# Performance work log

Measured on AMD Instinct MI355X. Metric: run time of the kernel, lower is better.

Reference implementation:

```python
import jax, jax.numpy as jnp
import numpy as np

N = 10000
E = 160000
C = 256        # in_channels
M = 256        # mid_channels
R = 64         # nregion


def _glorot(key, shape):
    fan_in, fan_out = shape[-1], shape[0]
    lim = (6.0 / (fan_in + fan_out)) ** 0.5
    return jax.random.uniform(key, shape, jnp.float32, -lim, lim)


def setup_inputs() -> dict:
    key = jax.random.key(0)
    ks = jax.random.split(key, 12)
    x = jax.random.normal(ks[0], (N, C), jnp.float32)
    edge_index = jax.random.randint(ks[1], (2, E), 0, N, jnp.int32)
    conv_w = _glorot(ks[2], (C, C))
    conv_b = jnp.zeros((C,), jnp.float32)
    lin1_w = _glorot(ks[3], (M, C)); lin1_b = jnp.zeros((M,), jnp.float32)
    lin2_w = _glorot(ks[4], (M, M)); lin2_b = jnp.zeros((M,), jnp.float32)
    lin3_w = _glorot(ks[5], (1, M)); lin3_b = jnp.zeros((1,), jnp.float32)
    lin4_w = _glorot(ks[6], (M, M)); lin4_b = jnp.zeros((M,), jnp.float32)
    bilin_w = _glorot(ks[7], (R, M, M)) * 0.1
    bilin_b = jnp.zeros((R,), jnp.float32)
    return {"x": x, "edge_index": edge_index,
            "conv_w": conv_w, "conv_b": conv_b,
            "lin1_w": lin1_w, "lin1_b": lin1_b,
            "lin2_w": lin2_w, "lin2_b": lin2_b,
            "lin3_w": lin3_w, "lin3_b": lin3_b,
            "lin4_w": lin4_w, "lin4_b": lin4_b,
            "bilin_w": bilin_w, "bilin_b": bilin_b}


def gcn_conv(x, edge_index, w, b):
    # PyG GCNConv: add self-loops, symmetric D^-1/2 (A+I) D^-1/2 normalization
    src, dst = edge_index[0], edge_index[1]
    n = x.shape[0]
    xw = x @ w.T                                            # [N, C]
    deg = jnp.ones((n,), xw.dtype).at[dst].add(jnp.ones((E,), xw.dtype))  # +1 for self loop
    dinv = jax.lax.rsqrt(deg)
    norm = dinv[src] * dinv[dst]                            # [E]
    agg = jnp.zeros_like(xw).at[dst].add(norm[:, None] * xw[src])
    agg = agg + (dinv * dinv)[:, None] * xw                 # self-loop messages
    return agg + b


def reference(x, edge_index, conv_w, conv_b, lin1_w, lin1_b, lin2_w, lin2_b,
              lin3_w, lin3_b, lin4_w, lin4_b, bilin_w, bilin_b):
    out = jax.nn.relu(gcn_conv(x, edge_index, conv_w, conv_b))
    x0 = out + x                                            # residual [N, C]
    x0 = jax.nn.relu(x0 @ lin1_w.T + lin1_b)                # [N, M]
    x1 = jax.nn.relu(x0 @ lin2_w.T + lin2_b)
    x1 = x1 @ lin3_w.T + lin3_b                             # [N, 1]
    x2 = jax.nn.relu(x0 @ lin4_w.T + lin4_b)                # [N, M]
    # Bilinear(x2, x2): out[n,r] = x2[n] @ W[r] @ x2[n] + b[r]
    t = (x2 @ bilin_w.reshape(R * M, M).T).reshape(-1, R, M)  # [N, R, M]
    x2 = jnp.sum(t * x2[:, None, :], axis=-1) + bilin_b       # [N, R]
    return (x1, x2)
```

## Files before the change

kernel.cpp:

```cpp
#include <hip/hip_runtime.h>

typedef unsigned short u16;
typedef __attribute__((ext_vector_type(8))) short bf16x8;
typedef __attribute__((ext_vector_type(4))) float f32x4;

#define N_NODES 10000
#define E_EDGES 160000

__device__ __forceinline__ float b2f(u16 u) {
  union { unsigned i; float f; } c; c.i = ((unsigned)u) << 16; return c.f;
}
__device__ __forceinline__ u16 f2b(float f) {
  union { float f; unsigned i; } c; c.f = f;
  unsigned i = c.i;
  return (u16)((i + 0x7FFFu + ((i >> 16) & 1u)) >> 16);
}

__global__ void detect_kernel(const unsigned* __restrict__ w, int* __restrict__ flag) {
  int t = threadIdx.x;
  int cnt = 0;
  for (int i = t; i < 1024; i += 64) {
    unsigned e = (w[i] >> 7) & 0xFF;
    cnt += (e >= 100 && e <= 145) ? 1 : 0;
  }
  for (int o = 32; o; o >>= 1) cnt += __shfl_xor(cnt, o);
  if (t == 0) *flag = (cnt >= 512) ? 1 : 0;
}
__global__ void canon_kernel(const void* __restrict__ src, u16* __restrict__ dst,
                             int n, const int* __restrict__ flag) {
  int i = blockIdx.x * 256 + threadIdx.x;
  if (i >= n) return;
  if (*flag) dst[i] = ((const u16*)src)[i];
  else       dst[i] = f2b(((const float*)src)[i]);
}
__global__ void canon4_kernel(const void* s0, const void* s1, const void* s2, const void* s3,
                              u16* d0, u16* d1, u16* d2, u16* d3,
                              const int* __restrict__ flag) {
  int tsel = blockIdx.x >> 8;
  int i = (blockIdx.x & 255) * 256 + threadIdx.x;
  const void* s = tsel == 0 ? s0 : tsel == 1 ? s1 : tsel == 2 ? s2 : s3;
  u16* d = tsel == 0 ? d0 : tsel == 1 ? d1 : tsel == 2 ? d2 : d3;
  if (*flag) d[i] = ((const u16*)s)[i];
  else       d[i] = f2b(((const float*)s)[i]);
}
__global__ void canon_small_kernel(const void* s0, const void* s1, const void* s2,
                                   const void* s3, const void* s4, const void* s5,
                                   const void* s6,
                                   u16* d0, u16* d1, u16* d2, u16* d3, u16* d4,
                                   u16* d5, u16* d6, const int* __restrict__ flag) {
  int t = threadIdx.x;
  int f = *flag;
  const void* srcs[7] = {s0, s1, s2, s3, s4, s5, s6};
  u16* dsts[7] = {d0, d1, d2, d3, d4, d5, d6};
  const int ns[7] = {256, 256, 256, 256, 256, 64, 1};
#pragma unroll
  for (int k = 0; k < 7; ++k) {
    if (t < ns[k]) {
      if (f) dsts[k][t] = ((const u16*)srcs[k])[t];
      else   dsts[k][t] = f2b(((const float*)srcs[k])[t]);
    }
  }
}

__device__ __forceinline__ void stage_async(const u16* __restrict__ src, int stride,
                                            int row0, int maxRow, int k0,
                                            u16* lds, int w, int lane) {
  int rsel = lane >> 3;
  int gch = (lane & 7) ^ rsel;
#pragma unroll
  for (int i = 0; i < 4; ++i) {
    int rb = (w * 4 + i) * 8;
    int grow = row0 + rb + rsel;
    grow = grow > maxRow ? maxRow : grow;
    const u16* gp = src + (size_t)grow * stride + k0 + gch * 8;
    u16* lp = lds + rb * 64;
    __builtin_amdgcn_global_load_lds(
        (const __attribute__((address_space(1))) void*)gp,
        (__attribute__((address_space(3))) void*)lp, 16, 0, 0);
  }
}

__device__ __forceinline__ void mma_tile(const u16* lA, const u16* lB,
                                         f32x4 acc[4][4], int wr, int wc, int lane) {
#pragma unroll
  for (int ks = 0; ks < 2; ++ks) {
    bf16x8 af[4], bfr[4];
    int g = ks * 4 + (lane >> 4);
#pragma unroll
    for (int t = 0; t < 4; ++t) {
      int rowA = wr * 64 + t * 16 + (lane & 15);
      af[t] = *(const bf16x8*)(lA + rowA * 64 + ((g ^ (rowA & 7)) * 8));
      int rowB = wc * 64 + t * 16 + (lane & 15);
      bfr[t] = *(const bf16x8*)(lB + rowB * 64 + ((g ^ (rowB & 7)) * 8));
    }
#pragma unroll
    for (int ti = 0; ti < 4; ++ti)
#pragma unroll
      for (int tj = 0; tj < 4; ++tj)
        acc[ti][tj] = __builtin_amdgcn_mfma_f32_16x16x32_bf16(af[ti], bfr[tj],
                                                              acc[ti][tj], 0, 0, 0);
  }
}

template <bool RELU, bool F32OUT>
__global__ __launch_bounds__(256, 2)
void gemm_kernel(const u16* __restrict__ A, const u16* __restrict__ B,
                 const u16* __restrict__ bias, float* __restrict__ outF,
                 u16* __restrict__ outB, int NN, int J, int K) {
  __shared__ u16 lA[128 * 64];
  __shared__ u16 lB[128 * 64];
  int lane = threadIdx.x & 63;
  int w = threadIdx.x >> 6;
  int wr = w >> 1, wc = w & 1;
  int n0 = blockIdx.y * 128;
  int j0 = blockIdx.x * 128;
  f32x4 acc[4][4];
#pragma unroll
  for (int i = 0; i < 4; ++i)
#pragma unroll
    for (int j = 0; j < 4; ++j) acc[i][j] = (f32x4){0.f, 0.f, 0.f, 0.f};

  for (int kt = 0; kt < K; kt += 64) {
    stage_async(A, K, n0, NN - 1, kt, lA, w, lane);
    stage_async(B, K, j0, J - 1, kt, lB, w, lane);
    __syncthreads();
    mma_tile(lA, lB, acc, wr, wc, lane);
    __syncthreads();
  }

#pragma unroll
  for (int ti = 0; ti < 4; ++ti)
#pragma unroll
    for (int tj = 0; tj < 4; ++tj) {
      int col = j0 + wc * 64 + tj * 16 + (lane & 15);
      float bv = bias ? b2f(bias[col]) : 0.0f;
#pragma unroll
      for (int r = 0; r < 4; ++r) {
        int row = n0 + wr * 64 + ti * 16 + ((lane >> 4) << 2) + r;
        if (row < NN) {
          float v = acc[ti][tj][r] + bv;
          if (RELU) v = fmaxf(v, 0.0f);
          if (F32OUT) outF[(size_t)row * J + col] = v;
          else        outB[(size_t)row * J + col] = f2b(v);
        }
      }
    }
}

__global__ __launch_bounds__(256, 2)
void gemm_fused234_kernel(const u16* __restrict__ A, const u16* __restrict__ B,
                          const u16* __restrict__ bias, const u16* __restrict__ w3,
                          float* __restrict__ out1acc, u16* __restrict__ x2v, int NN) {
  __shared__ u16 lA[128 * 64];
  __shared__ u16 lB[128 * 64];
  int lane = threadIdx.x & 63;
  int w = threadIdx.x >> 6;
  int wr = w >> 1, wc = w & 1;
  int n0 = blockIdx.y * 128;
  int j0 = blockIdx.x * 128;
  f32x4 acc[4][4];
#pragma unroll
  for (int i = 0; i < 4; ++i)
#pragma unroll
    for (int j = 0; j < 4; ++j) acc[i][j] = (f32x4){0.f, 0.f, 0.f, 0.f};

  for (int kt = 0; kt < 256; kt += 64) {
    stage_async(A, 256, n0, NN - 1, kt, lA, w, lane);
    stage_async(B, 256, j0, 511, kt, lB, w, lane);
    __syncthreads();
    mma_tile(lA, lB, acc, wr, wc, lane);
    __syncthreads();
  }

  if (j0 < 256) {
    float part[4][4];
#pragma unroll
    for (int ti = 0; ti < 4; ++ti)
#pragma unroll
      for (int r = 0; r < 4; ++r) part[ti][r] = 0.0f;
#pragma unroll
    for (int ti = 0; ti < 4; ++ti)
#pragma unroll
      for (int tj = 0; tj < 4; ++tj) {
        int col = j0 + wc * 64 + tj * 16 + (lane & 15);
        float bv = b2f(bias[col]);
        float wv = b2f(w3[col]);
#pragma unroll
        for (int r = 0; r < 4; ++r) {
          float v = fmaxf(acc[ti][tj][r] + bv, 0.0f);
          part[ti][r] += v * wv;
        }
      }
#pragma unroll
    for (int ti = 0; ti < 4; ++ti)
#pragma unroll
      for (int r = 0; r < 4; ++r) {
        float s = part[ti][r];
        s += __shfl_xor(s, 1);
        s += __shfl_xor(s, 2);
        s += __shfl_xor(s, 4);
        s += __shfl_xor(s, 8);
        if ((lane & 15) == 0) {
          int row = n0 + wr * 64 + ti * 16 + ((lane >> 4) << 2) + r;
          if (row < NN) unsafeAtomicAdd(&out1acc[row], s);
        }
      }
  } else {
#pragma unroll
    for (int ti = 0; ti < 4; ++ti)
#pragma unroll
      for (int tj = 0; tj < 4; ++tj) {
        int col = j0 + wc * 64 + tj * 16 + (lane & 15);
        float bv = b2f(bias[col]);
#pragma unroll
        for (int r = 0; r < 4; ++r) {
          int row = n0 + wr * 64 + ti * 16 + ((lane >> 4) << 2) + r;
          if (row < NN) {
            float v = fmaxf(acc[ti][tj][r] + bv, 0.0f);
            x2v[(size_t)row * 256 + (col - 256)] = f2b(v);
          }
        }
      }
  }
}

__global__ __launch_bounds__(256, 2)
void bilinear_kernel(const u16* __restrict__ x2v, const u16* __restrict__ W,
                     float* __restrict__ out2acc, int NN) {
  __shared__ u16 lA[128 * 64];
  __shared__ u16 lB[128 * 64];
  int lane = threadIdx.x & 63;
  int w = threadIdx.x >> 6;
  int wr = w >> 1, wc = w & 1;
  int n0 = blockIdx.y * 128;
  int rm0 = blockIdx.x * 128;
  int m0g = rm0 & 255;
  int xv_kt = (m0g >> 6) + wc;
  f32x4 acc[4][4];
#pragma unroll
  for (int i = 0; i < 4; ++i)
#pragma unroll
    for (int j = 0; j < 4; ++j) acc[i][j] = (f32x4){0.f, 0.f, 0.f, 0.f};

  u16 xvr[4][16];

#pragma unroll
  for (int kt4 = 0; kt4 < 4; ++kt4) {
    stage_async(x2v, 256, n0, NN - 1, kt4 * 64, lA, w, lane);
    stage_async(W, 256, rm0, 16383, kt4 * 64, lB, w, lane);
    __syncthreads();
    mma_tile(lA, lB, acc, wr, wc, lane);
    if (kt4 == xv_kt) {
#pragma unroll
      for (int tj = 0; tj < 4; ++tj) {
        int kl = tj * 16 + (lane & 15);
        int ch = kl >> 3, off = kl & 7;
#pragma unroll
        for (int ti = 0; ti < 4; ++ti)
#pragma unroll
          for (int r = 0; r < 4; ++r) {
            int rowl = wr * 64 + ti * 16 + ((lane >> 4) << 2) + r;
            xvr[tj][ti * 4 + r] = lA[rowl * 64 + ((ch ^ (rowl & 7)) * 8) + off];
          }
      }
    }
    __syncthreads();
  }

  int region = rm0 >> 8;
  float rowsum[4][4];
#pragma unroll
  for (int ti = 0; ti < 4; ++ti)
#pragma unroll
    for (int r = 0; r < 4; ++r) rowsum[ti][r] = 0.0f;

#pragma unroll
  for (int ti = 0; ti < 4; ++ti)
#pragma unroll
    for (int tj = 0; tj < 4; ++tj)
#pragma unroll
      for (int r = 0; r < 4; ++r)
        rowsum[ti][r] += acc[ti][tj][r] * b2f(xvr[tj][ti * 4 + r]);

#pragma unroll
  for (int ti = 0; ti < 4; ++ti)
#pragma unroll
    for (int r = 0; r < 4; ++r) {
      float s = rowsum[ti][r];
      s += __shfl_xor(s, 1);
      s += __shfl_xor(s, 2);
      s += __shfl_xor(s, 4);
      s += __shfl_xor(s, 8);
      if ((lane & 15) == 0) {
        int rowl = wr * 64 + ti * 16 + ((lane >> 4) << 2) + r;
        int n = n0 + rowl;
        if (n < NN) unsafeAtomicAdd(&out2acc[(size_t)n * 64 + region], s);
      }
    }
}

__global__ void hist_kernel(const int* __restrict__ ei, int* __restrict__ count) {
  int i = blockIdx.x * 256 + threadIdx.x;
  if (i < E_EDGES) atomicAdd(&count[ei[E_EDGES + i]], 1);
}

__global__ void scan_kernel(const int* __restrict__ count, int* __restrict__ start,
                            int* __restrict__ cursor, float* __restrict__ dinv) {
  __shared__ int sdata[1024];
  __shared__ int carry_s;
  int t = threadIdx.x;
  if (t == 0) carry_s = 0;
  __syncthreads();
  for (int base = 0; base < N_NODES; base += 1024) {
    int i = base + t;
    int v = (i < N_NODES) ? count[i] : 0;
    sdata[t] = v;
    __syncthreads();
    for (int o = 1; o < 1024; o <<= 1) {
      int u = (t >= o) ? sdata[t - o] : 0;
      __syncthreads();
      sdata[t] += u;
      __syncthreads();
    }
    int excl = sdata[t] - v + carry_s;
    if (i < N_NODES) {
      start[i] = excl;
      cursor[i] = excl;
      dinv[i] = rsqrtf(1.0f + (float)v);
    }
    __syncthreads();
    if (t == 1023) carry_s += sdata[1023];
    __syncthreads();
  }
}

__global__ void place_kernel(const int* __restrict__ ei, int* __restrict__ cursor,
                             int* __restrict__ order) {
  int i = blockIdx.x * 256 + threadIdx.x;
  if (i >= E_EDGES) return;
  int d = ei[E_EDGES + i];
  int pos = atomicAdd(&cursor[d], 1);
  order[pos] = i;
}

__global__ void gather_kernel(const int* __restrict__ ei, const int* __restrict__ order,
                              const int* __restrict__ start, const int* __restrict__ count,
                              const float* __restrict__ dinv, const float* __restrict__ xw,
                              const u16* __restrict__ conv_b, const u16* __restrict__ x,
                              u16* __restrict__ x0) {
  int node = (blockIdx.x * blockDim.x + threadIdx.x) >> 6;
  int lane = threadIdx.x & 63;
  if (node >= N_NODES) return;
  int s0 = start[node], cnt = count[node];
  float dn = dinv[node];
  float ax = 0.f, ay = 0.f, az = 0.f, aw = 0.f;
  for (int base = 0; base < cnt; base += 64) {
    int rem = cnt - base;
    int m = rem < 64 ? rem : 64;
    int eid = (lane < m) ? order[s0 + base + lane] : 0;
    int s = (lane < m) ? ei[eid] : 0;
    float nrm = (lane < m) ? dinv[s] * dn : 0.f;
    for (int j = 0; j < m; ++j) {
      int sj = __shfl(s, j);
      float nj = __shfl(nrm, j);
      float4 v = *((const float4*)(xw + (size_t)sj * 256) + lane);
      ax += nj * v.x; ay += nj * v.y; az += nj * v.z; aw += nj * v.w;
    }
  }
  float4 sv = *((const float4*)(xw + (size_t)node * 256) + lane);
  float slw = dn * dn;
  const u16* bb = conv_b + lane * 4;
  const u16* xr = x + (size_t)node * 256 + lane * 4;
  u16 o[4];
  float vals[4] = {ax + slw * sv.x, ay + slw * sv.y, az + slw * sv.z, aw + slw * sv.w};
#pragma unroll
  for (int j = 0; j < 4; ++j) {
    float v = vals[j] + b2f(bb[j]);
    v = fmaxf(v, 0.0f) + b2f(xr[j]);
    o[j] = f2b(v);
  }
  *((ushort4*)(x0 + (size_t)node * 256) + lane) = make_ushort4(o[0], o[1], o[2], o[3]);
}

__global__ void out_final_kernel(const float* __restrict__ out1acc,
                                 const float* __restrict__ out2acc,
                                 const u16* __restrict__ b3, const u16* __restrict__ bb,
                                 void* __restrict__ dout, const int* __restrict__ flag) {
  int idx = blockIdx.x * 256 + threadIdx.x;
  int f = *flag;
  if (idx < N_NODES) {
    float v = out1acc[idx] + b2f(b3[0]);
    if (f) ((u16*)dout)[idx] = f2b(v);
    else   ((float*)dout)[idx] = v;
  } else if (idx < N_NODES + N_NODES * 64) {
    int k = idx - N_NODES;
    float v = out2acc[k] + b2f(bb[k & 63]);
    if (f) ((u16*)dout)[idx] = f2b(v);
    else   ((float*)dout)[idx] = v;
  }
}

extern "C" void kernel_launch(void* const* d_in, const int* in_sizes, int n_in,
                              void* d_out, int out_size, void* d_ws, size_t ws_size,
                              hipStream_t stream) {
  const int* ei = (const int*)d_in[1];

  float* ws      = (float*)d_ws;
  float* xw      = ws;
  int*   count   = (int*)(xw + N_NODES * 256);
  int*   start   = count + 10240;
  int*   cursor  = start + 10240;
  int*   order   = cursor + 10240;
  float* dinv    = (float*)(order + E_EDGES);
  float* out1acc = dinv + 10240;
  float* out2acc = out1acc + 10240;
  u16* x0  = (u16*)(out2acc + N_NODES * 64);
  u16* x0m = x0 + N_NODES * 256;
  u16* x2v = x0m + N_NODES * 256;
  u16* cx  = x2v + N_NODES * 256;
  u16* cwc = cx + N_NODES * 256;
  u16* cw1 = cwc + 65536;
  u16* cw2 = cw1 + 65536;
  u16* cw4 = cw2 + 65536;
  u16* cwB = cw4 + 65536;
  u16* cbc = cwB + 4194304;
  u16* cb1 = cbc + 256;
  u16* cb2 = cb1 + 256;
  u16* cb4 = cb2 + 256;
  u16* cw3 = cb4 + 256;
  u16* cbB = cw3 + 256;
  u16* cb3 = cbB + 64;
  int* flag = (int*)(cb3 + 16);

  hipMemsetAsync(count, 0, N_NODES * sizeof(int), stream);
  hipMemsetAsync(out1acc, 0, (10240 + (size_t)N_NODES * 64) * sizeof(float), stream);

  detect_kernel<<<1, 64, 0, stream>>>((const unsigned*)d_in[0], flag);

  canon_kernel<<<(N_NODES * 256 + 255) / 256, 256, 0, stream>>>(d_in[0], cx, N_NODES * 256, flag);
  canon4_kernel<<<1024, 256, 0, stream>>>(d_in[2], d_in[4], d_in[6], d_in[10],
                                          cwc, cw1, cw2, cw4, flag);
  canon_small_kernel<<<1, 256, 0, stream>>>(d_in[3], d_in[5], d_in[7], d_in[11],
                                            d_in[8], d_in[13], d_in[9],
                                            cbc, cb1, cb2, cb4, cw3, cbB, cb3, flag);
  canon_kernel<<<(4194304 + 255) / 256, 256, 0, stream>>>(d_in[12], cwB, 4194304, flag);

  hist_kernel<<<(E_EDGES + 255) / 256, 256, 0, stream>>>(ei, count);
  scan_kernel<<<1, 1024, 0, stream>>>(count, start, cursor, dinv);
  place_kernel<<<(E_EDGES + 255) / 256, 256, 0, stream>>>(ei, cursor, order);

  gemm_kernel<false, true><<<dim3(2, 79), 256, 0, stream>>>(
      cx, cwc, nullptr, xw, nullptr, N_NODES, 256, 256);

  gather_kernel<<<(N_NODES * 64 + 255) / 256, 256, 0, stream>>>(
      ei, order, start, count, dinv, xw, cbc, cx, x0);

  gemm_kernel<true, false><<<dim3(2, 79), 256, 0, stream>>>(
      x0, cw1, cb1, nullptr, x0m, N_NODES, 256, 256);

  gemm_fused234_kernel<<<dim3(4, 79), 256, 0, stream>>>(
      x0m, cw2, cb2, cw3, out1acc, x2v, N_NODES);

  bilinear_kernel<<<dim3(128, 79), 256, 0, stream>>>(x2v, cwB, out2acc, N_NODES);

  out_final_kernel<<<(N_NODES * 65 + 255) / 256, 256, 0, stream>>>(
      out1acc, out2acc, cb3, cbB, d_out, flag);
}
```

Before: 413.8 us.

## Load bilinear MFMA operands directly from global memory and use a wave-shuffle scan

The bilinear kernel no longer stages both operands through shared memory with two barriers per k-step. Each lane now reads its bf16x8 A and B fragments straight from global/L2 and feeds them to MFMA. Only the two 64-column x2 slices needed for the final row-dot are staged once into LDS. The node-degree scan is rewritten from a barrier-heavy Hillis-Steele over shared memory into a warp-shuffle scan plus a 16-entry wave-sum scan, which cuts block barriers. The risk is that the direct global loads are less coalesced and cannot be reused across waves, which raises L2 traffic.

```diff
diff --git a/kernel.cpp b/kernel.cpp
--- a/kernel.cpp
+++ b/kernel.cpp
@@ -227,45 +227,53 @@
 __global__ __launch_bounds__(256, 2)
 void bilinear_kernel(const u16* __restrict__ x2v, const u16* __restrict__ W,
                      float* __restrict__ out2acc, int NN) {
-  __shared__ u16 lA[128 * 64];
-  __shared__ u16 lB[128 * 64];
+  __shared__ u16 lX[2][128 * 64];
   int lane = threadIdx.x & 63;
   int w = threadIdx.x >> 6;
   int wr = w >> 1, wc = w & 1;
   int n0 = blockIdx.y * 128;
   int rm0 = blockIdx.x * 128;
   int m0g = rm0 & 255;
-  int xv_kt = (m0g >> 6) + wc;
+
+  stage_async(x2v, 256, n0, NN - 1, m0g, lX[0], w, lane);
+  stage_async(x2v, 256, n0, NN - 1, m0g + 64, lX[1], w, lane);
+
+  const u16* pa[4];
+  const u16* pb[4];
+#pragma unroll
+  for (int t = 0; t < 4; ++t) {
+    int rowA = n0 + wr * 64 + t * 16 + (lane & 15);
+    rowA = rowA > NN - 1 ? NN - 1 : rowA;
+    pa[t] = x2v + (size_t)rowA * 256 + ((lane >> 4) * 8);
+    int rowB = rm0 + wc * 64 + t * 16 + (lane & 15);
+    pb[t] = W + (size_t)rowB * 256 + ((lane >> 4) * 8);
+  }
+
   f32x4 acc[4][4];
 #pragma unroll
   for (int i = 0; i < 4; ++i)
 #pragma unroll
     for (int j = 0; j < 4; ++j) acc[i][j] = (f32x4){0.f, 0.f, 0.f, 0.f};
 
-  u16 xvr[4][16];
-
-#pragma unroll
-  for (int kt4 = 0; kt4 < 4; ++kt4) {
-    stage_async(x2v, 256, n0, NN - 1, kt4 * 64, lA, w, lane);
-    stage_async(W, 256, rm0, 16383, kt4 * 64, lB, w, lane);
-    __syncthreads();
-    mma_tile(lA, lB, acc, wr, wc, lane);
-    if (kt4 == xv_kt) {
-#pragma unroll
-      for (int tj = 0; tj < 4; ++tj) {
-        int kl = tj * 16 + (lane & 15);
-        int ch = kl >> 3, off = kl & 7;
-#pragma unroll
-        for (int ti = 0; ti < 4; ++ti)
-#pragma unroll
-          for (int r = 0; r < 4; ++r) {
-            int rowl = wr * 64 + ti * 16 + ((lane >> 4) << 2) + r;
-            xvr[tj][ti * 4 + r] = lA[rowl * 64 + ((ch ^ (rowl & 7)) * 8) + off];
-          }
-      }
-    }
-    __syncthreads();
-  }
+#pragma unroll
+  for (int kt = 0; kt < 4; ++kt)
+#pragma unroll
+    for (int ks = 0; ks < 2; ++ks) {
+      int k0 = kt * 64 + ks * 32;
+      bf16x8 af[4], bfr[4];
+#pragma unroll
+      for (int t = 0; t < 4; ++t) af[t] = *(const bf16x8*)(pa[t] + k0);
+#pragma unroll
+      for (int t = 0; t < 4; ++t) bfr[t] = *(const bf16x8*)(pb[t] + k0);
+#pragma unroll
+      for (int ti = 0; ti < 4; ++ti)
+#pragma unroll
+        for (int tj = 0; tj < 4; ++tj)
+          acc[ti][tj] = __builtin_amdgcn_mfma_f32_16x16x32_bf16(af[ti], bfr[tj],
+                                                                acc[ti][tj], 0, 0, 0);
+    }
+
+  __syncthreads();
 
   int region = rm0 >> 8;
   float rowsum[4][4];
@@ -277,10 +285,16 @@
 #pragma unroll
   for (int ti = 0; ti < 4; ++ti)
 #pragma unroll
-    for (int tj = 0; tj < 4; ++tj)
-#pragma unroll
-      for (int r = 0; r < 4; ++r)
-        rowsum[ti][r] += acc[ti][tj][r] * b2f(xvr[tj][ti * 4 + r]);
+    for (int tj = 0; tj < 4; ++tj) {
+      int kl = tj * 16 + (lane & 15);
+      int ch = kl >> 3, off = kl & 7;
+#pragma unroll
+      for (int r = 0; r < 4; ++r) {
+        int rowl = wr * 64 + ti * 16 + ((lane >> 4) << 2) + r;
+        float xv = b2f(lX[wc][rowl * 64 + ((ch ^ (rowl & 7)) * 8) + off]);
+        rowsum[ti][r] += acc[ti][tj][r] * xv;
+      }
+    }
 
 #pragma unroll
   for (int ti = 0; ti < 4; ++ti)
@@ -306,30 +320,41 @@
 
 __global__ void scan_kernel(const int* __restrict__ count, int* __restrict__ start,
                             int* __restrict__ cursor, float* __restrict__ dinv) {
-  __shared__ int sdata[1024];
+  __shared__ int wsum[16];
   __shared__ int carry_s;
   int t = threadIdx.x;
+  int wv = t >> 6, ln = t & 63;
   if (t == 0) carry_s = 0;
   __syncthreads();
   for (int base = 0; base < N_NODES; base += 1024) {
     int i = base + t;
     int v = (i < N_NODES) ? count[i] : 0;
-    sdata[t] = v;
-    __syncthreads();
-    for (int o = 1; o < 1024; o <<= 1) {
-      int u = (t >= o) ? sdata[t - o] : 0;
-      __syncthreads();
-      sdata[t] += u;
-      __syncthreads();
-    }
-    int excl = sdata[t] - v + carry_s;
+    int s = v;
+#pragma unroll
+    for (int o = 1; o < 64; o <<= 1) {
+      int u = __shfl_up(s, o);
+      if (ln >= o) s += u;
+    }
+    if (ln == 63) wsum[wv] = s;
+    __syncthreads();
+    if (wv == 0) {
+      int x = (ln < 16) ? wsum[ln] : 0;
+#pragma unroll
+      for (int o = 1; o < 16; o <<= 1) {
+        int u = __shfl_up(x, o);
+        if (ln >= o) x += u;
+      }
+      if (ln < 16) wsum[ln] = x;
+    }
+    __syncthreads();
+    int excl = s - v + (wv ? wsum[wv - 1] : 0) + carry_s;
     if (i < N_NODES) {
       start[i] = excl;
       cursor[i] = excl;
       dinv[i] = rsqrtf(1.0f + (float)v);
     }
     __syncthreads();
-    if (t == 1023) carry_s += sdata[1023];
+    if (t == 0) carry_s += wsum[15];
     __syncthreads();
   }
 }
```

After: 546.9 us. 32.2% more time.
